# Performance work log

Hardware: AMD Instinct MI355X
Metric: run time of the kernel (lower is better)

## Reference

```python
import jax, jax.numpy as jnp
import numpy as np

N_NODES = 100000
N_EDGES = 3200000
N_GRAPHS = 2048
D = 256
ATOM_VOCAB = 100
BOND_VOCAB = 10
EPS = 1e-5


def setup_inputs() -> dict:
    key = jax.random.key(0)
    ks = jax.random.split(key, 20)
    inp = {
        "x": jax.random.randint(ks[0], (N_NODES, 9), 0, ATOM_VOCAB),
        "edge_index": jax.random.randint(ks[1], (2, N_EDGES), 0, N_NODES),
        "edge_attr": jax.random.randint(ks[2], (N_EDGES, 3), 0, BOND_VOCAB),
        "batch": jnp.sort(jax.random.randint(ks[3], (N_NODES,), 0, N_GRAPHS)),
        # embedding tables (OGB-style: one table per categorical column, summed)
        "atom_emb": jax.random.normal(ks[4], (9, ATOM_VOCAB, D)) * 0.02,
        "bond_emb1": jax.random.normal(ks[5], (3, BOND_VOCAB, D)) * 0.02,
        "bond_emb2": jax.random.normal(ks[6], (3, BOND_VOCAB, D)) * 0.02,
        # conv1 MLP: Linear(D,2D) -> BN -> ReLU -> Linear(2D,D) -> ReLU
        "c1_w1": jax.random.normal(ks[7], (D, 2 * D)) * (1.0 / np.sqrt(D)),
        "c1_b1": jnp.zeros((2 * D,)),
        "c1_g": jnp.ones((2 * D,)),
        "c1_be": jnp.zeros((2 * D,)),
        "c1_w2": jax.random.normal(ks[8], (2 * D, D)) * (1.0 / np.sqrt(2 * D)),
        "c1_b2": jnp.zeros((D,)),
        # conv2 MLP: Linear(D,D) -> BN -> ReLU -> Linear(D,D) -> ReLU
        "c2_w1": jax.random.normal(ks[9], (D, D)) * (1.0 / np.sqrt(D)),
        "c2_b1": jnp.zeros((D,)),
        "c2_g": jnp.ones((D,)),
        "c2_be": jnp.zeros((D,)),
        "c2_w2": jax.random.normal(ks[10], (D, D)) * (1.0 / np.sqrt(D)),
        "c2_b2": jnp.zeros((D,)),
    }
    return inp


def _batchnorm(z, g, b):
    # BatchNorm1d in training mode: batch statistics over the node axis
    mu = jnp.mean(z, axis=0)
    var = jnp.var(z, axis=0)
    return (z - mu) * jax.lax.rsqrt(var + EPS) * g + b


def _bond_encode(tables, edge_attr):
    # sum of per-column embeddings: [E,3] -> [E,D]
    return jnp.sum(tables[jnp.arange(3)[None, :], edge_attr], axis=1)


def _gin_conv(h, edge_index, e_emb, w1, b1, g, be, w2, b2):
    src, dst = edge_index[0], edge_index[1]
    # message: relu(x_j + edge_emb), aggregate: scatter-add at dst
    m = jax.nn.relu(h[src] + e_emb)                       # [E, D]
    agg = jax.ops.segment_sum(m, dst, num_segments=h.shape[0])
    z = agg + h
    z = jax.nn.relu(_batchnorm(z @ w1 + b1, g, be))
    return jax.nn.relu(z @ w2 + b2)


def reference(x, edge_index, edge_attr, batch,
              atom_emb, bond_emb1, bond_emb2,
              c1_w1, c1_b1, c1_g, c1_be, c1_w2, c1_b2,
              c2_w1, c2_b1, c2_g, c2_be, c2_w2, c2_b2):
    # AtomEncoder: sum of 9 per-column embeddings -> [N, D]
    h = jnp.sum(atom_emb[jnp.arange(9)[None, :], x], axis=1)
    e1 = _bond_encode(bond_emb1, edge_attr)
    h = _gin_conv(h, edge_index, e1, c1_w1, c1_b1, c1_g, c1_be, c1_w2, c1_b2)
    h = jax.nn.relu(h)
    e2 = _bond_encode(bond_emb2, edge_attr)
    h = _gin_conv(h, edge_index, e2, c2_w1, c2_b1, c2_g, c2_be, c2_w2, c2_b2)
    h = jax.nn.relu(h)
    # global add pool over graphs
    return jax.ops.segment_sum(h, batch, num_segments=N_GRAPHS)
```

## Files before the change

kernel.cpp:

```cpp
#include <hip/hip_runtime.h>

#define NN 100000
#define NE 3200000
#define NG 2048
#define DD 256
#define EPSV 1e-5f
#define SCAN_N 100096
#define SCAN_B 391
#define GCH 1568
#define NGCH 64

typedef unsigned int uint32;
typedef __attribute__((ext_vector_type(2))) unsigned int uivec2;
typedef __attribute__((ext_vector_type(4))) unsigned int uivec4;
typedef __attribute__((ext_vector_type(4))) float f32x4;
typedef __attribute__((ext_vector_type(8))) short short8_t;

__device__ __forceinline__ float4 ld4(const float* p) {
    return *reinterpret_cast<const float4*>(p);
}
__device__ __forceinline__ void st4(float* p, float4 v) {
    *reinterpret_cast<float4*>(p) = v;
}
__device__ __forceinline__ uivec4 ldu4(const uint32* p) {
    return *reinterpret_cast<const uivec4*>(p);
}

__device__ __forceinline__ uint32 packsplit(float x) {
    uint32 u = __float_as_uint(x);
    uint32 hb = u >> 16;
    float hf = __uint_as_float(hb << 16);
    float lo = x - hf;
    uint32 lb = __float_as_uint(lo) >> 16;
    return hb | (lb << 16);
}
__device__ __forceinline__ float unpacksplit(uint32 u) {
    return __uint_as_float(u << 16) + __uint_as_float(u & 0xffff0000u);
}

__global__ __launch_bounds__(256) void zero_k(float* __restrict__ p, int n) {
    int i = blockIdx.x * 256 + threadIdx.x;
    if (i < n) p[i] = 0.f;
}

__global__ __launch_bounds__(256) void packmat_k(const float* __restrict__ X,
                                                 uint32* __restrict__ Xp, int n) {
    int i = blockIdx.x * 256 + threadIdx.x;
    if (i < n) Xp[i] = packsplit(X[i]);
}

__global__ __launch_bounds__(256) void atom_embed_k(
    const int* __restrict__ x, const float* __restrict__ emb,
    uint32* __restrict__ Hp)
{
    int lane = threadIdx.x & 63;
    int n = blockIdx.x * 4 + (threadIdx.x >> 6);
    if (n >= NN) return;
    int c4 = lane * 4;
    float4 acc = make_float4(0.f, 0.f, 0.f, 0.f);
#pragma unroll
    for (int c = 0; c < 9; ++c) {
        int idx = x[n * 9 + c];
        float4 v = ld4(emb + (size_t)(c * 100 + idx) * DD + c4);
        acc.x += v.x; acc.y += v.y; acc.z += v.z; acc.w += v.w;
    }
    uivec4 o;
    o[0] = packsplit(acc.x); o[1] = packsplit(acc.y);
    o[2] = packsplit(acc.z); o[3] = packsplit(acc.w);
    *reinterpret_cast<uivec4*>(Hp + (size_t)n * DD + c4) = o;
}

__global__ __launch_bounds__(256) void bcomb_k(const float* __restrict__ bond,
                                               float* __restrict__ bcomb)
{
    int combo = blockIdx.x;
    int col = threadIdx.x;
    int b0 = combo % 10, b1 = (combo / 10) % 10, b2 = combo / 100;
    bcomb[(size_t)combo * DD + col] =
        bond[(size_t)b0 * DD + col] +
        bond[(size_t)(10 + b1) * DD + col] +
        bond[(size_t)(20 + b2) * DD + col];
}

__global__ __launch_bounds__(256) void hist_k(const int* __restrict__ ei,
                                              int* __restrict__ cnt)
{
    int e = blockIdx.x * 256 + threadIdx.x;
    if (e < NE) atomicAdd(&cnt[ei[NE + e]], 1);
}

__global__ __launch_bounds__(256) void scan1_k(int* __restrict__ cnt,
                                               int* __restrict__ bsum)
{
    __shared__ int s[2][256];
    int t = threadIdx.x;
    int i = blockIdx.x * 256 + t;
    int v = cnt[i];
    s[0][t] = v;
    __syncthreads();
    int p = 0;
    for (int off = 1; off < 256; off <<= 1) {
        int xv = s[p][t];
        if (t >= off) xv += s[p][t - off];
        s[p ^ 1][t] = xv;
        p ^= 1;
        __syncthreads();
    }
    int inc = s[p][t];
    cnt[i] = inc - v;
    if (t == 255) bsum[blockIdx.x] = inc;
}

__global__ __launch_bounds__(512) void scan2_k(const int* __restrict__ bsum,
                                               int* __restrict__ boff)
{
    __shared__ int s[2][512];
    int t = threadIdx.x;
    int v = (t < SCAN_B) ? bsum[t] : 0;
    s[0][t] = v;
    __syncthreads();
    int p = 0;
    for (int off = 1; off < 512; off <<= 1) {
        int xv = s[p][t];
        if (t >= off) xv += s[p][t - off];
        s[p ^ 1][t] = xv;
        p ^= 1;
        __syncthreads();
    }
    boff[t] = s[p][t] - v;
}

__global__ __launch_bounds__(256) void scan3_k(const int* __restrict__ cnt,
                                               const int* __restrict__ boff,
                                               int* __restrict__ rs,
                                               int* __restrict__ cursor)
{
    int i = blockIdx.x * 256 + threadIdx.x;
    int v = cnt[i] + boff[blockIdx.x];
    rs[i] = v;
    if (i < NN) cursor[i] = v;
}

__global__ __launch_bounds__(256) void scatter_k(const int* __restrict__ ei,
                                                 const int* __restrict__ ea,
                                                 int* __restrict__ cursor,
                                                 int* __restrict__ meta)
{
    int e = blockIdx.x * 256 + threadIdx.x;
    if (e >= NE) return;
    int src = ei[e];
    int dst = ei[NE + e];
    int combo = ea[e * 3 + 0] + 10 * ea[e * 3 + 1] + 100 * ea[e * 3 + 2];
    int pos = atomicAdd(&cursor[dst], 1);
    meta[pos] = (src << 10) | combo;
}

__device__ __forceinline__ void edge_acc2(const uint32* __restrict__ Hp,
                                          const float* __restrict__ bcomb,
                                          int m, int c2, float& ax, float& ay)
{
    uivec2 v = *reinterpret_cast<const uivec2*>(Hp + (size_t)(m >> 10) * DD + c2);
    float2 b = *reinterpret_cast<const float2*>(bcomb + (size_t)(m & 1023) * DD + c2);
    ax += fmaxf(unpacksplit(v[0]) + b.x, 0.f);
    ay += fmaxf(unpacksplit(v[1]) + b.y, 0.f);
}

__global__ __launch_bounds__(256) void gather_half_k(
    const uint32* __restrict__ Hp, const float* __restrict__ bcomb,
    const int* __restrict__ rs, const int* __restrict__ meta,
    uint32* __restrict__ Zp, int colbase)
{
    int lane = threadIdx.x & 63;
    int n = blockIdx.x * 4 + (threadIdx.x >> 6);
    if (n >= NN) return;
    int c2 = colbase + lane * 2;
    uivec2 hu = *reinterpret_cast<const uivec2*>(Hp + (size_t)n * DD + c2);
    float ax = unpacksplit(hu[0]), ay = unpacksplit(hu[1]);
    int lo = rs[n], hi = rs[n + 1];
    int t = lo;
    for (; t + 4 <= hi; t += 4) {
        int m0 = meta[t], m1 = meta[t + 1], m2 = meta[t + 2], m3 = meta[t + 3];
        edge_acc2(Hp, bcomb, m0, c2, ax, ay);
        edge_acc2(Hp, bcomb, m1, c2, ax, ay);
        edge_acc2(Hp, bcomb, m2, c2, ax, ay);
        edge_acc2(Hp, bcomb, m3, c2, ax, ay);
    }
    for (; t < hi; ++t)
        edge_acc2(Hp, bcomb, meta[t], c2, ax, ay);
    uivec2 z;
    z[0] = packsplit(ax); z[1] = packsplit(ay);
    *reinterpret_cast<uivec2*>(Zp + (size_t)n * DD + c2) = z;
}

__global__ __launch_bounds__(256) void gram_mfma_k(const uint32* __restrict__ Zp,
                                                   float* __restrict__ G)
{
    __shared__ uint32 Ta[32][130];
    __shared__ uint32 Tb[32][130];
    const int tid = threadIdx.x;
    const int lane = tid & 63;
    const int l15 = lane & 15;
    const int l4 = lane >> 4;
    const int wave = tid >> 6;
    const int wm = wave >> 1, wn = wave & 1;
    const int bj = blockIdx.x & 1;
    const int bi = (blockIdx.x >> 1) & 1;
    const int ch = blockIdx.x >> 2;
    const int rbase = ch * GCH;

    f32x4 acc[4][4] = {};

    for (int kt = 0; kt < GCH; kt += 32) {
        __syncthreads();
#pragma unroll
        for (int i = 0; i < 4; ++i) {
            int f = i * 256 + tid;
            int row = f >> 5, cq = f & 31;
            int r = rbase + kt + row;
            uivec4 a = {0, 0, 0, 0}, b = {0, 0, 0, 0};
            if (r < NN) {
                a = ldu4(Zp + (size_t)r * DD + bi * 128 + cq * 4);
                b = ldu4(Zp + (size_t)r * DD + bj * 128 + cq * 4);
            }
            *reinterpret_cast<uivec4*>(&Ta[row][cq * 4]) = a;
            *reinterpret_cast<uivec4*>(&Tb[row][cq * 4]) = b;
        }
        __syncthreads();

        short8_t ah[4], al[4], bh[4], bl[4];
#pragma unroll
        for (int mi = 0; mi < 4; ++mi) {
            int ci = wm * 64 + mi * 16 + l15;
            short8_t h, l;
#pragma unroll
            for (int j = 0; j < 8; ++j) {
                uint32 u = Ta[l4 * 8 + j][ci];
                h[j] = (short)(u & 0xffff);
                l[j] = (short)(u >> 16);
            }
            ah[mi] = h; al[mi] = l;
        }
#pragma unroll
        for (int ni = 0; ni < 4; ++ni) {
            int ci = wn * 64 + ni * 16 + l15;
            short8_t h, l;
#pragma unroll
            for (int j = 0; j < 8; ++j) {
                uint32 u = Tb[l4 * 8 + j][ci];
                h[j] = (short)(u & 0xffff);
                l[j] = (short)(u >> 16);
            }
            bh[ni] = h; bl[ni] = l;
        }
#pragma unroll
        for (int mi = 0; mi < 4; ++mi)
#pragma unroll
            for (int ni = 0; ni < 4; ++ni) {
                acc[mi][ni] = __builtin_amdgcn_mfma_f32_16x16x32_bf16(ah[mi], bh[ni], acc[mi][ni], 0, 0, 0);
                acc[mi][ni] = __builtin_amdgcn_mfma_f32_16x16x32_bf16(ah[mi], bl[ni], acc[mi][ni], 0, 0, 0);
                acc[mi][ni] = __builtin_amdgcn_mfma_f32_16x16x32_bf16(al[mi], bh[ni], acc[mi][ni], 0, 0, 0);
            }
    }

#pragma unroll
    for (int mi = 0; mi < 4; ++mi) {
#pragma unroll
        for (int ni = 0; ni < 4; ++ni) {
            int col = bj * 128 + wn * 64 + ni * 16 + l15;
#pragma unroll
            for (int r = 0; r < 4; ++r) {
                int row = bi * 128 + wm * 64 + mi * 16 + l4 * 4 + r;
                atomicAdd(&G[row * 256 + col], acc[mi][ni][r]);
            }
        }
    }
}

__global__ __launch_bounds__(256) void colsum_k(const uint32* __restrict__ Zp,
                                                float* __restrict__ cs)
{
    int t = threadIdx.x;
    int r0 = blockIdx.x * 256;
    int r1 = r0 + 256 < NN ? r0 + 256 : NN;
    float acc = 0.f;
    for (int r = r0; r < r1; ++r) acc += unpacksplit(Zp[(size_t)r * DD + t]);
    atomicAdd(&cs[t], acc);
}

__global__ __launch_bounds__(256) void bnprep_k(
    const float* __restrict__ G, const float* __restrict__ cs,
    const float* __restrict__ W, const float* __restrict__ b,
    const float* __restrict__ g, const float* __restrict__ be,
    float* __restrict__ scl, float* __restrict__ shf, int N)
{
    __shared__ float wv[256];
    __shared__ double r1[256];
    __shared__ double r2[256];
    int c = blockIdx.x;
    int t = threadIdx.x;
    wv[t] = W[t * N + c];
    __syncthreads();
    double gd = 0.0;
    const float* Gr = G + t * 256;
    for (int j = 0; j < 256; ++j) gd += (double)Gr[j] * (double)wv[j];
    r1[t] = (double)wv[t] * gd;
    r2[t] = (double)cs[t] * (double)wv[t];
    __syncthreads();
    for (int off = 128; off > 0; off >>= 1) {
        if (t < off) { r1[t] += r1[t + off]; r2[t] += r2[t + off]; }
        __syncthreads();
    }
    if (t == 0) {
        double szw = r2[0];
        double s2zw = r1[0];
        double bb = (double)b[c];
        double fN = (double)NN;
        double S1 = szw + fN * bb;
        double S2 = s2zw + 2.0 * bb * szw + fN * bb * bb;
        double mu = S1 / fN;
        double var = S2 / fN - mu * mu;
        float s = g[c] * rsqrtf((float)var + EPSV);
        scl[c] = s;
        shf[c] = be[c] - (float)mu * s;
    }
}

template <int OUTM>
__global__ __launch_bounds__(256) void gemm_mfma_k(
    const uint32* __restrict__ Ap, const uint32* __restrict__ Wp,
    const float* __restrict__ bias, uint32* __restrict__ Cp,
    int M, int N, int K,
    const float* __restrict__ scl, const float* __restrict__ shf)
{
    __shared__ uint32 As[128][36];

    const int tid = threadIdx.x;
    const int lane = tid & 63;
    const int l15 = lane & 15;
    const int l4 = lane >> 4;
    const int wave = tid >> 6;
    const int wm = wave >> 1, wn = wave & 1;
    const int ntx = N / 128;
    const int bx = blockIdx.x % ntx;
    const int by = blockIdx.x / ntx;
    const int row0 = by * 128, col0 = bx * 128;

    f32x4 acc[4][4] = {};

    for (int kt = 0; kt < K; kt += 32) {
        __syncthreads();
#pragma unroll
        for (int i = 0; i < 4; ++i) {
            int f = i * 256 + tid;
            int row = f >> 3, q = f & 7;
            int r = row0 + row;
            if (r >= M) r = M - 1;
            *reinterpret_cast<uivec4*>(&As[row][q * 4]) =
                ldu4(Ap + (size_t)r * K + kt + q * 4);
        }
        __syncthreads();

        short8_t ah[4], al[4];
#pragma unroll
        for (int mi = 0; mi < 4; ++mi) {
            int m = wm * 64 + mi * 16 + l15;
            uivec4 u0 = *reinterpret_cast<const uivec4*>(&As[m][l4 * 8]);
            uivec4 u1 = *reinterpret_cast<const uivec4*>(&As[m][l4 * 8 + 4]);
            short8_t h, l;
#pragma unroll
            for (int j = 0; j < 4; ++j) {
                h[j] = (short)(u0[j] & 0xffff);
                l[j] = (short)(u0[j] >> 16);
                h[4 + j] = (short)(u1[j] & 0xffff);
                l[4 + j] = (short)(u1[j] >> 16);
            }
            ah[mi] = h; al[mi] = l;
        }
        short8_t bh[4], bl[4];
#pragma unroll
        for (int ni = 0; ni < 4; ++ni) {
            int col = col0 + wn * 64 + ni * 16 + l15;
            const uint32* wp = Wp + (size_t)(kt + l4 * 8) * N + col;
            short8_t h, l;
#pragma unroll
            for (int j = 0; j < 8; ++j) {
                uint32 u = wp[(size_t)j * N];
                h[j] = (short)(u & 0xffff);
                l[j] = (short)(u >> 16);
            }
            bh[ni] = h; bl[ni] = l;
        }
#pragma unroll
        for (int mi = 0; mi < 4; ++mi)
#pragma unroll
            for (int ni = 0; ni < 4; ++ni) {
                acc[mi][ni] = __builtin_amdgcn_mfma_f32_16x16x32_bf16(ah[mi], bh[ni], acc[mi][ni], 0, 0, 0);
                acc[mi][ni] = __builtin_amdgcn_mfma_f32_16x16x32_bf16(ah[mi], bl[ni], acc[mi][ni], 0, 0, 0);
                acc[mi][ni] = __builtin_amdgcn_mfma_f32_16x16x32_bf16(al[mi], bh[ni], acc[mi][ni], 0, 0, 0);
            }
    }

#pragma unroll
    for (int ni = 0; ni < 4; ++ni) {
        int col = col0 + wn * 64 + ni * 16 + l15;
        float bv = bias[col];
        float sc = 0.f, sh = 0.f;
        if constexpr (OUTM == 2) { sc = scl[col]; sh = shf[col]; }
#pragma unroll
        for (int mi = 0; mi < 4; ++mi) {
#pragma unroll
            for (int r = 0; r < 4; ++r) {
                int row = row0 + wm * 64 + mi * 16 + l4 * 4 + r;
                if (row < M) {
                    float v = acc[mi][ni][r] + bv;
                    if constexpr (OUTM == 2) v = fmaf(v, sc, sh);
                    v = fmaxf(v, 0.f);
                    Cp[(size_t)row * N + col] = packsplit(v);
                }
            }
        }
    }
}

__device__ __forceinline__ int lower_bound_i(const int* a, int n, int key) {
    int lo = 0, hi = n;
    while (lo < hi) {
        int mid = (lo + hi) >> 1;
        if (a[mid] < key) lo = mid + 1; else hi = mid;
    }
    return lo;
}

__global__ __launch_bounds__(256) void pool_k(
    const uint32* __restrict__ Hp, const int* __restrict__ batch,
    float* __restrict__ out)
{
    int g = blockIdx.x;
    int col = threadIdx.x;
    int lo = lower_bound_i(batch, NN, g);
    int hi = lower_bound_i(batch, NN, g + 1);
    float acc = 0.f;
    for (int n = lo; n < hi; ++n) acc += unpacksplit(Hp[(size_t)n * DD + col]);
    out[(size_t)g * DD + col] = acc;
}

extern "C" void kernel_launch(void* const* d_in, const int* in_sizes, int n_in,
                              void* d_out, int out_size, void* d_ws, size_t ws_size,
                              hipStream_t stream)
{
    const int*   x        = (const int*)d_in[0];
    const int*   ei       = (const int*)d_in[1];
    const int*   ea       = (const int*)d_in[2];
    const int*   batch    = (const int*)d_in[3];
    const float* atom_emb = (const float*)d_in[4];
    const float* bond1    = (const float*)d_in[5];
    const float* bond2    = (const float*)d_in[6];
    const float* c1_w1    = (const float*)d_in[7];
    const float* c1_b1    = (const float*)d_in[8];
    const float* c1_g     = (const float*)d_in[9];
    const float* c1_be    = (const float*)d_in[10];
    const float* c1_w2    = (const float*)d_in[11];
    const float* c1_b2    = (const float*)d_in[12];
    const float* c2_w1    = (const float*)d_in[13];
    const float* c2_b1    = (const float*)d_in[14];
    const float* c2_g     = (const float*)d_in[15];
    const float* c2_be    = (const float*)d_in[16];
    const float* c2_w2    = (const float*)d_in[17];
    const float* c2_b2    = (const float*)d_in[18];
    float* out = (float*)d_out;

    uint32* Hp   = (uint32*)d_ws;
    uint32* Zp   = Hp + (size_t)NN * DD;
    float*  G    = (float*)(Zp + (size_t)NN * DD);
    float*  cs   = G + 65536;
    float*  scl  = cs + 256;
    float*  shf  = scl + 512;
    float*  bcomb = shf + 512;
    uint32* W1p = (uint32*)(bcomb + 1000 * DD);
    uint32* W2p = W1p + 256 * 512;
    uint32* W3p = W2p + 512 * 256;
    uint32* W4p = W3p + 256 * 256;
    int* cnt    = (int*)(W4p + 256 * 256);
    int* rs     = cnt + SCAN_N;
    int* bsum   = rs + SCAN_N;
    int* boff   = bsum + 512;
    int* cursor = boff + 512;
    int* meta   = cursor + NN;
    uint32* ystrip = (uint32*)(meta + NE);

    size_t fixed_bytes = (size_t)((char*)ystrip - (char*)d_ws);
    size_t avail = ws_size > fixed_bytes ? ws_size - fixed_bytes : 0;
    int strip = (int)(avail / (512 * sizeof(uint32)));
    strip = (strip / 128) * 128;
    if (strip > 25600) strip = 25600;
    if (strip < 128) strip = 128;

    const int eb = (NE + 255) / 256;

    zero_k<<<(SCAN_N + 255) / 256, 256, 0, stream>>>((float*)cnt, SCAN_N);
    zero_k<<<(65792 + 255) / 256, 256, 0, stream>>>(G, 65792);

    packmat_k<<<512, 256, 0, stream>>>(c1_w1, W1p, 256 * 512);
    packmat_k<<<512, 256, 0, stream>>>(c1_w2, W2p, 512 * 256);
    packmat_k<<<256, 256, 0, stream>>>(c2_w1, W3p, 256 * 256);
    packmat_k<<<256, 256, 0, stream>>>(c2_w2, W4p, 256 * 256);

    atom_embed_k<<<NN / 4, 256, 0, stream>>>(x, atom_emb, Hp);

    hist_k<<<eb, 256, 0, stream>>>(ei, cnt);
    scan1_k<<<SCAN_B, 256, 0, stream>>>(cnt, bsum);
    scan2_k<<<1, 512, 0, stream>>>(bsum, boff);
    scan3_k<<<SCAN_B, 256, 0, stream>>>(cnt, boff, rs, cursor);
    scatter_k<<<eb, 256, 0, stream>>>(ei, ea, cursor, meta);

    bcomb_k<<<1000, 256, 0, stream>>>(bond1, bcomb);
    gather_half_k<<<NN / 4, 256, 0, stream>>>(Hp, bcomb, rs, meta, Zp, 0);
    gather_half_k<<<NN / 4, 256, 0, stream>>>(Hp, bcomb, rs, meta, Zp, 128);
    gram_mfma_k<<<4 * NGCH, 256, 0, stream>>>(Zp, G);
    colsum_k<<<SCAN_B, 256, 0, stream>>>(Zp, cs);
    bnprep_k<<<512, 256, 0, stream>>>(G, cs, c1_w1, c1_b1, c1_g, c1_be, scl, shf, 512);
    for (int r0 = 0; r0 < NN; r0 += strip) {
        int Ms = (NN - r0 < strip) ? NN - r0 : strip;
        int mt = (Ms + 127) / 128;
        gemm_mfma_k<2><<<mt * 4, 256, 0, stream>>>(
            Zp + (size_t)r0 * DD, W1p, c1_b1, ystrip, Ms, 512, 256, scl, shf);
        gemm_mfma_k<1><<<mt * 2, 256, 0, stream>>>(
            ystrip, W2p, c1_b2, Hp + (size_t)r0 * DD, Ms, 256, 512, nullptr, nullptr);
    }

    zero_k<<<(65792 + 255) / 256, 256, 0, stream>>>(G, 65792);
    bcomb_k<<<1000, 256, 0, stream>>>(bond2, bcomb);
    gather_half_k<<<NN / 4, 256, 0, stream>>>(Hp, bcomb, rs, meta, Zp, 0);
    gather_half_k<<<NN / 4, 256, 0, stream>>>(Hp, bcomb, rs, meta, Zp, 128);
    gram_mfma_k<<<4 * NGCH, 256, 0, stream>>>(Zp, G);
    colsum_k<<<SCAN_B, 256, 0, stream>>>(Zp, cs);
    bnprep_k<<<256, 256, 0, stream>>>(G, cs, c2_w1, c2_b1, c2_g, c2_be, scl, shf, 256);
    for (int r0 = 0; r0 < NN; r0 += strip) {
        int Ms = (NN - r0 < strip) ? NN - r0 : strip;
        int mt = (Ms + 127) / 128;
        gemm_mfma_k<2><<<mt * 2, 256, 0, stream>>>(
            Zp + (size_t)r0 * DD, W3p, c2_b1, ystrip, Ms, 256, 256, scl, shf);
        gemm_mfma_k<1><<<mt * 2, 256, 0, stream>>>(
            ystrip, W4p, c2_b2, Hp + (size_t)r0 * DD, Ms, 256, 256, nullptr, nullptr);
    }

    pool_k<<<NG, 256, 0, stream>>>(Hp, batch, out);
}
```

Baseline: 2.486 ms.

## Split packed bf16 hi/lo activations into separate planes; gather only hi half

Activations stored as interleaved hi/lo bf16 pairs in one uint32 array are split into two separate bf16 planes. The edge gather reads only the high plane for neighbour features, halving random-gather bytes, and processes all 256 columns in one pass instead of two half passes. packsplit now rounds to nearest for the high part so the hi-only message stays reasonably accurate. The cost is lower precision in messages (bf16 instead of split fp32), extra repacking when the planes are loaded into GEMM shared memory, and a larger strip cap.

```diff
diff --git a/kernel.cpp b/kernel.cpp
--- a/kernel.cpp
+++ b/kernel.cpp
@@ -11,32 +11,27 @@
 #define NGCH 64
 
 typedef unsigned int uint32;
-typedef __attribute__((ext_vector_type(2))) unsigned int uivec2;
+typedef unsigned short ushort16;
 typedef __attribute__((ext_vector_type(4))) unsigned int uivec4;
+typedef __attribute__((ext_vector_type(4))) unsigned short usvec4;
 typedef __attribute__((ext_vector_type(4))) float f32x4;
 typedef __attribute__((ext_vector_type(8))) short short8_t;
 
 __device__ __forceinline__ float4 ld4(const float* p) {
     return *reinterpret_cast<const float4*>(p);
 }
-__device__ __forceinline__ void st4(float* p, float4 v) {
-    *reinterpret_cast<float4*>(p) = v;
-}
-__device__ __forceinline__ uivec4 ldu4(const uint32* p) {
-    return *reinterpret_cast<const uivec4*>(p);
+__device__ __forceinline__ float bf2f(ushort16 b) {
+    return __uint_as_float((uint32)b << 16);
 }
 
 __device__ __forceinline__ uint32 packsplit(float x) {
     uint32 u = __float_as_uint(x);
-    uint32 hb = u >> 16;
+    uint32 hb = (u + 0x7fffu + ((u >> 16) & 1u)) >> 16;
     float hf = __uint_as_float(hb << 16);
     float lo = x - hf;
     uint32 lb = __float_as_uint(lo) >> 16;
     return hb | (lb << 16);
 }
-__device__ __forceinline__ float unpacksplit(uint32 u) {
-    return __uint_as_float(u << 16) + __uint_as_float(u & 0xffff0000u);
-}
 
 __global__ __launch_bounds__(256) void zero_k(float* __restrict__ p, int n) {
     int i = blockIdx.x * 256 + threadIdx.x;
@@ -51,7 +46,7 @@
 
 __global__ __launch_bounds__(256) void atom_embed_k(
     const int* __restrict__ x, const float* __restrict__ emb,
-    uint32* __restrict__ Hp)
+    ushort16* __restrict__ Hh, ushort16* __restrict__ Hl)
 {
     int lane = threadIdx.x & 63;
     int n = blockIdx.x * 4 + (threadIdx.x >> 6);
@@ -64,10 +59,16 @@
         float4 v = ld4(emb + (size_t)(c * 100 + idx) * DD + c4);
         acc.x += v.x; acc.y += v.y; acc.z += v.z; acc.w += v.w;
     }
-    uivec4 o;
-    o[0] = packsplit(acc.x); o[1] = packsplit(acc.y);
-    o[2] = packsplit(acc.z); o[3] = packsplit(acc.w);
-    *reinterpret_cast<uivec4*>(Hp + (size_t)n * DD + c4) = o;
+    float a[4] = {acc.x, acc.y, acc.z, acc.w};
+    usvec4 h, l;
+#pragma unroll
+    for (int j = 0; j < 4; ++j) {
+        uint32 u = packsplit(a[j]);
+        h[j] = (ushort16)(u & 0xffff);
+        l[j] = (ushort16)(u >> 16);
+    }
+    *reinterpret_cast<usvec4*>(Hh + (size_t)n * DD + c4) = h;
+    *reinterpret_cast<usvec4*>(Hl + (size_t)n * DD + c4) = l;
 }
 
 __global__ __launch_bounds__(256) void bcomb_k(const float* __restrict__ bond,
@@ -155,45 +156,61 @@
     meta[pos] = (src << 10) | combo;
 }
 
-__device__ __forceinline__ void edge_acc2(const uint32* __restrict__ Hp,
-                                          const float* __restrict__ bcomb,
-                                          int m, int c2, float& ax, float& ay)
-{
-    uivec2 v = *reinterpret_cast<const uivec2*>(Hp + (size_t)(m >> 10) * DD + c2);
-    float2 b = *reinterpret_cast<const float2*>(bcomb + (size_t)(m & 1023) * DD + c2);
-    ax += fmaxf(unpacksplit(v[0]) + b.x, 0.f);
-    ay += fmaxf(unpacksplit(v[1]) + b.y, 0.f);
-}
-
-__global__ __launch_bounds__(256) void gather_half_k(
-    const uint32* __restrict__ Hp, const float* __restrict__ bcomb,
+__device__ __forceinline__ void edge_acc(const ushort16* __restrict__ Hh,
+                                         const float* __restrict__ bcomb,
+                                         int m, int c4,
+                                         float& a0, float& a1, float& a2, float& a3)
+{
+    usvec4 v = *reinterpret_cast<const usvec4*>(Hh + (size_t)(m >> 10) * DD + c4);
+    float4 b = ld4(bcomb + (size_t)(m & 1023) * DD + c4);
+    a0 += fmaxf(bf2f(v[0]) + b.x, 0.f);
+    a1 += fmaxf(bf2f(v[1]) + b.y, 0.f);
+    a2 += fmaxf(bf2f(v[2]) + b.z, 0.f);
+    a3 += fmaxf(bf2f(v[3]) + b.w, 0.f);
+}
+
+__global__ __launch_bounds__(256) void gather_full_k(
+    const ushort16* __restrict__ Hh, const ushort16* __restrict__ Hl,
+    const float* __restrict__ bcomb,
     const int* __restrict__ rs, const int* __restrict__ meta,
-    uint32* __restrict__ Zp, int colbase)
+    ushort16* __restrict__ Zh, ushort16* __restrict__ Zl)
 {
     int lane = threadIdx.x & 63;
     int n = blockIdx.x * 4 + (threadIdx.x >> 6);
     if (n >= NN) return;
-    int c2 = colbase + lane * 2;
-    uivec2 hu = *reinterpret_cast<const uivec2*>(Hp + (size_t)n * DD + c2);
-    float ax = unpacksplit(hu[0]), ay = unpacksplit(hu[1]);
+    int c4 = lane * 4;
+    usvec4 sh = *reinterpret_cast<const usvec4*>(Hh + (size_t)n * DD + c4);
+    usvec4 sl = *reinterpret_cast<const usvec4*>(Hl + (size_t)n * DD + c4);
+    float a0 = bf2f(sh[0]) + bf2f(sl[0]);
+    float a1 = bf2f(sh[1]) + bf2f(sl[1]);
+    float a2 = bf2f(sh[2]) + bf2f(sl[2]);
+    float a3 = bf2f(sh[3]) + bf2f(sl[3]);
     int lo = rs[n], hi = rs[n + 1];
     int t = lo;
     for (; t + 4 <= hi; t += 4) {
         int m0 = meta[t], m1 = meta[t + 1], m2 = meta[t + 2], m3 = meta[t + 3];
-        edge_acc2(Hp, bcomb, m0, c2, ax, ay);
-        edge_acc2(Hp, bcomb, m1, c2, ax, ay);
-        edge_acc2(Hp, bcomb, m2, c2, ax, ay);
-        edge_acc2(Hp, bcomb, m3, c2, ax, ay);
+        edge_acc(Hh, bcomb, m0, c4, a0, a1, a2, a3);
+        edge_acc(Hh, bcomb, m1, c4, a0, a1, a2, a3);
+        edge_acc(Hh, bcomb, m2, c4, a0, a1, a2, a3);
+        edge_acc(Hh, bcomb, m3, c4, a0, a1, a2, a3);
     }
     for (; t < hi; ++t)
-        edge_acc2(Hp, bcomb, meta[t], c2, ax, ay);
-    uivec2 z;
-    z[0] = packsplit(ax); z[1] = packsplit(ay);
-    *reinterpret_cast<uivec2*>(Zp + (size_t)n * DD + c2) = z;
-}
-
-__global__ __launch_bounds__(256) void gram_mfma_k(const uint32* __restrict__ Zp,
-                                                   float* __restrict__ G)
+        edge_acc(Hh, bcomb, meta[t], c4, a0, a1, a2, a3);
+    float a[4] = {a0, a1, a2, a3};
+    usvec4 zh, zl;
+#pragma unroll
+    for (int j = 0; j < 4; ++j) {
+        uint32 u = packsplit(a[j]);
+        zh[j] = (ushort16)(u & 0xffff);
+        zl[j] = (ushort16)(u >> 16);
+    }
+    *reinterpret_cast<usvec4*>(Zh + (size_t)n * DD + c4) = zh;
+    *reinterpret_cast<usvec4*>(Zl + (size_t)n * DD + c4) = zl;
+}
+
+__global__ __launch_bounds__(256) void gram_mfma_k(
+    const ushort16* __restrict__ Zh, const ushort16* __restrict__ Zl,
+    float* __restrict__ G)
 {
     __shared__ uint32 Ta[32][130];
     __shared__ uint32 Tb[32][130];
@@ -215,15 +232,24 @@
 #pragma unroll
         for (int i = 0; i < 4; ++i) {
             int f = i * 256 + tid;
-            int row = f >> 5, cq = f & 31;
+            int row = f >> 5, g4 = f & 31;
             int r = rbase + kt + row;
-            uivec4 a = {0, 0, 0, 0}, b = {0, 0, 0, 0};
+            uivec4 pa = {0, 0, 0, 0}, pb = {0, 0, 0, 0};
             if (r < NN) {
-                a = ldu4(Zp + (size_t)r * DD + bi * 128 + cq * 4);
-                b = ldu4(Zp + (size_t)r * DD + bj * 128 + cq * 4);
-            }
-            *reinterpret_cast<uivec4*>(&Ta[row][cq * 4]) = a;
-            *reinterpret_cast<uivec4*>(&Tb[row][cq * 4]) = b;
+                const ushort16* zh = Zh + (size_t)r * DD;
+                const ushort16* zl = Zl + (size_t)r * DD;
+                usvec4 ah_ = *reinterpret_cast<const usvec4*>(zh + bi * 128 + g4 * 4);
+                usvec4 al_ = *reinterpret_cast<const usvec4*>(zl + bi * 128 + g4 * 4);
+                usvec4 bh_ = *reinterpret_cast<const usvec4*>(zh + bj * 128 + g4 * 4);
+                usvec4 bl_ = *reinterpret_cast<const usvec4*>(zl + bj * 128 + g4 * 4);
+#pragma unroll
+                for (int j = 0; j < 4; ++j) {
+                    pa[j] = (uint32)ah_[j] | ((uint32)al_[j] << 16);
+                    pb[j] = (uint32)bh_[j] | ((uint32)bl_[j] << 16);
+                }
+            }
+            *reinterpret_cast<uivec4*>(&Ta[row][g4 * 4]) = pa;
+            *reinterpret_cast<uivec4*>(&Tb[row][g4 * 4]) = pb;
         }
         __syncthreads();
 
@@ -276,14 +302,16 @@
     }
 }
 
-__global__ __launch_bounds__(256) void colsum_k(const uint32* __restrict__ Zp,
+__global__ __launch_bounds__(256) void colsum_k(const ushort16* __restrict__ Zh,
+                                                const ushort16* __restrict__ Zl,
                                                 float* __restrict__ cs)
 {
     int t = threadIdx.x;
     int r0 = blockIdx.x * 256;
     int r1 = r0 + 256 < NN ? r0 + 256 : NN;
     float acc = 0.f;
-    for (int r = r0; r < r1; ++r) acc += unpacksplit(Zp[(size_t)r * DD + t]);
+    for (int r = r0; r < r1; ++r)
+        acc += bf2f(Zh[(size_t)r * DD + t]) + bf2f(Zl[(size_t)r * DD + t]);
     atomicAdd(&cs[t], acc);
 }
 
@@ -327,8 +355,9 @@
 
 template <int OUTM>
 __global__ __launch_bounds__(256) void gemm_mfma_k(
-    const uint32* __restrict__ Ap, const uint32* __restrict__ Wp,
-    const float* __restrict__ bias, uint32* __restrict__ Cp,
+    const ushort16* __restrict__ Ah, const ushort16* __restrict__ Al,
+    const uint32* __restrict__ Wp, const float* __restrict__ bias,
+    ushort16* __restrict__ Ch, ushort16* __restrict__ Cl,
     int M, int N, int K,
     const float* __restrict__ scl, const float* __restrict__ shf)
 {
@@ -355,8 +384,13 @@
             int row = f >> 3, q = f & 7;
             int r = row0 + row;
             if (r >= M) r = M - 1;
-            *reinterpret_cast<uivec4*>(&As[row][q * 4]) =
-                ldu4(Ap + (size_t)r * K + kt + q * 4);
+            usvec4 hh = *reinterpret_cast<const usvec4*>(Ah + (size_t)r * K + kt + q * 4);
+            usvec4 ll = *reinterpret_cast<const usvec4*>(Al + (size_t)r * K + kt + q * 4);
+            uivec4 pk;
+#pragma unroll
+            for (int j = 0; j < 4; ++j)
+                pk[j] = (uint32)hh[j] | ((uint32)ll[j] << 16);
+            *reinterpret_cast<uivec4*>(&As[row][q * 4]) = pk;
         }
         __syncthreads();
 
@@ -415,7 +449,9 @@
                     float v = acc[mi][ni][r] + bv;
                     if constexpr (OUTM == 2) v = fmaf(v, sc, sh);
                     v = fmaxf(v, 0.f);
-                    Cp[(size_t)row * N + col] = packsplit(v);
+                    uint32 u = packsplit(v);
+                    Ch[(size_t)row * N + col] = (ushort16)(u & 0xffff);
+                    Cl[(size_t)row * N + col] = (ushort16)(u >> 16);
                 }
             }
         }
@@ -432,15 +468,16 @@
 }
 
 __global__ __launch_bounds__(256) void pool_k(
-    const uint32* __restrict__ Hp, const int* __restrict__ batch,
-    float* __restrict__ out)
+    const ushort16* __restrict__ Hh, const ushort16* __restrict__ Hl,
+    const int* __restrict__ batch, float* __restrict__ out)
 {
     int g = blockIdx.x;
     int col = threadIdx.x;
     int lo = lower_bound_i(batch, NN, g);
     int hi = lower_bound_i(batch, NN, g + 1);
     float acc = 0.f;
-    for (int n = lo; n < hi; ++n) acc += unpacksplit(Hp[(size_t)n * DD + col]);
+    for (int n = lo; n < hi; ++n)
+        acc += bf2f(Hh[(size_t)n * DD + col]) + bf2f(Hl[(size_t)n * DD + col]);
     out[(size_t)g * DD + col] = acc;
 }
 
@@ -469,9 +506,11 @@
     const float* c2_b2    = (const float*)d_in[18];
     float* out = (float*)d_out;
 
-    uint32* Hp   = (uint32*)d_ws;
-    uint32* Zp   = Hp + (size_t)NN * DD;
-    float*  G    = (float*)(Zp + (size_t)NN * DD);
+    ushort16* Hh = (ushort16*)d_ws;
+    ushort16* Hl = Hh + (size_t)NN * DD;
+    ushort16* Zh = Hl + (size_t)NN * DD;
+    ushort16* Zl = Zh + (size_t)NN * DD;
+    float*  G    = (float*)(Zl + (size_t)NN * DD);
     float*  cs   = G + 65536;
     float*  scl  = cs + 256;
     float*  shf  = scl + 512;
@@ -486,14 +525,16 @@
     int* boff   = bsum + 512;
     int* cursor = boff + 512;
     int* meta   = cursor + NN;
-    uint32* ystrip = (uint32*)(meta + NE);
-
-    size_t fixed_bytes = (size_t)((char*)ystrip - (char*)d_ws);
+    char* ybase = (char*)(meta + NE);
+
+    size_t fixed_bytes = (size_t)(ybase - (char*)d_ws);
     size_t avail = ws_size > fixed_bytes ? ws_size - fixed_bytes : 0;
-    int strip = (int)(avail / (512 * sizeof(uint32)));
+    int strip = (int)(avail / 2048);
     strip = (strip / 128) * 128;
-    if (strip > 25600) strip = 25600;
+    if (strip > 50048) strip = 50048;
     if (strip < 128) strip = 128;
+    ushort16* ysh = (ushort16*)ybase;
+    ushort16* ysl = ysh + (size_t)strip * 512;
 
     const int eb = (NE + 255) / 256;
 
@@ -505,7 +546,7 @@
     packmat_k<<<256, 256, 0, stream>>>(c2_w1, W3p, 256 * 256);
     packmat_k<<<256, 256, 0, stream>>>(c2_w2, W4p, 256 * 256);
 
-    atom_embed_k<<<NN / 4, 256, 0, stream>>>(x, atom_emb, Hp);
+    atom_embed_k<<<NN / 4, 256, 0, stream>>>(x, atom_emb, Hh, Hl);
 
     hist_k<<<eb, 256, 0, stream>>>(ei, cnt);
     scan1_k<<<SCAN_B, 256, 0, stream>>>(cnt, bsum);
@@ -514,35 +555,37 @@
     scatter_k<<<eb, 256, 0, stream>>>(ei, ea, cursor, meta);
 
     bcomb_k<<<1000, 256, 0, stream>>>(bond1, bcomb);
-    gather_half_k<<<NN / 4, 256, 0, stream>>>(Hp, bcomb, rs, meta, Zp, 0);
-    gather_half_k<<<NN / 4, 256, 0, stream>>>(Hp, bcomb, rs, meta, Zp, 128);
-    gram_mfma_k<<<4 * NGCH, 256, 0, stream>>>(Zp, G);
-    colsum_k<<<SCAN_B, 256, 0, stream>>>(Zp, cs);
+    gather_full_k<<<NN / 4, 256, 0, stream>>>(Hh, Hl, bcomb, rs, meta, Zh, Zl);
+    gram_mfma_k<<<4 * NGCH, 256, 0, stream>>>(Zh, Zl, G);
+    colsum_k<<<SCAN_B, 256, 0, stream>>>(Zh, Zl, cs);
     bnprep_k<<<512, 256, 0, stream>>>(G, cs, c1_w1, c1_b1, c1_g, c1_be, scl, shf, 512);
     for (int r0 = 0; r0 < NN; r0 += strip) {
         int Ms = (NN - r0 < strip) ? NN - r0 : strip;
         int mt = (Ms + 127) / 128;
         gemm_mfma_k<2><<<mt * 4, 256, 0, stream>>>(
-            Zp + (size_t)r0 * DD, W1p, c1_b1, ystrip, Ms, 512, 256, scl, shf);
+            Zh + (size_t)r0 * DD, Zl + (size_t)r0 * DD, W1p, c1_b1,
+            ysh, ysl, Ms, 512, 256, scl, shf);
         gemm_mfma_k<1><<<mt * 2, 256, 0, stream>>>(
-            ystrip, W2p, c1_b2, Hp + (size_t)r0 * DD, Ms, 256, 512, nullptr, nullptr);
+            ysh, ysl, W2p, c1_b2,
+            Hh + (size_t)r0 * DD, Hl + (size_t)r0 * DD, Ms, 256, 512, nullptr, nullptr);
     }
 
     zero_k<<<(65792 + 255) / 256, 256, 0, stream>>>(G, 65792);
     bcomb_k<<<1000, 256, 0, stream>>>(bond2, bcomb);
-    gather_half_k<<<NN / 4, 256, 0, stream>>>(Hp, bcomb, rs, meta, Zp, 0);
-    gather_half_k<<<NN / 4, 256, 0, stream>>>(Hp, bcomb, rs, meta, Zp, 128);
-    gram_mfma_k<<<4 * NGCH, 256, 0, stream>>>(Zp, G);
-    colsum_k<<<SCAN_B, 256, 0, stream>>>(Zp, cs);
+    gather_full_k<<<NN / 4, 256, 0, stream>>>(Hh, Hl, bcomb, rs, meta, Zh, Zl);
+    gram_mfma_k<<<4 * NGCH, 256, 0, stream>>>(Zh, Zl, G);
+    colsum_k<<<SCAN_B, 256, 0, stream>>>(Zh, Zl, cs);
     bnprep_k<<<256, 256, 0, stream>>>(G, cs, c2_w1, c2_b1, c2_g, c2_be, scl, shf, 256);
     for (int r0 = 0; r0 < NN; r0 += strip) {
         int Ms = (NN - r0 < strip) ? NN - r0 : strip;
         int mt = (Ms + 127) / 128;
         gemm_mfma_k<2><<<mt * 2, 256, 0, stream>>>(
-            Zp + (size_t)r0 * DD, W3p, c2_b1, ystrip, Ms, 256, 256, scl, shf);
+            Zh + (size_t)r0 * DD, Zl + (size_t)r0 * DD, W3p, c2_b1,
+            ysh, ysl, Ms, 256, 256, scl, shf);
         gemm_mfma_k<1><<<mt * 2, 256, 0, stream>>>(
-            ystrip, W4p, c2_b2, Hp + (size_t)r0 * DD, Ms, 256, 256, nullptr, nullptr);
-    }
-
-    pool_k<<<NG, 256, 0, stream>>>(Hp, batch, out);
-}
+            ysh, ysl, W4p, c2_b2,
+            Hh + (size_t)r0 * DD, Hl + (size_t)r0 * DD, Ms, 256, 256, nullptr, nullptr);
+    }
+
+    pool_k<<<NG, 256, 0, stream>>>(Hh, Hl, batch, out);
+}
```

New measurement: 2.306 ms. 7.2% less time.
